# Performance work log

Measured on AMD Instinct MI355X. Metric: run time of the kernel, lower is better.

## Reference

```python
import jax, jax.numpy as jnp
import numpy as np

H = 2048      # hidden_size
K = 16        # n_memory_tokens
NQ = K + 2    # extraction queries (+halt, +value)
NH = 4        # extraction heads
HD = H // NH  # head dim = 512
FFN = 2 * H   # ffn_mult=2
MAXE = 128    # memory buffer capacity (full -> eviction path)
B, S = 4, 4096
EPS = 1e-6


def setup_inputs() -> dict:
    key = jax.random.key(0)
    ks = jax.random.split(key, 20)
    r = lambda i, shape, s=0.02: jax.random.normal(ks[i], shape, jnp.float32) * s
    return {
        "hidden_states": jax.random.normal(ks[0], (B, S, H), jnp.float32),
        "buf_entries": jax.random.normal(ks[1], (MAXE, H), jnp.float32),
        "buf_priorities": jax.random.uniform(ks[2], (MAXE,), jnp.float32),
        "queries": r(3, (NQ, H)),
        "Wq": r(4, (H, H)), "Wk": r(5, (H, H)), "Wv": r(6, (H, H)), "Wo": r(7, (H, H)),
        "ln_w": jnp.ones((H,), jnp.float32),
        "Wgate": r(8, (FFN, H)), "Wup": r(9, (FFN, H)), "Wdown": r(10, (H, FFN)),
        "Wp": r(11, (1, H)), "bp": jnp.full((1,), 0.5, jnp.float32),
        "Wh": r(12, (1, H)), "bh": jnp.full((1,), 1.0, jnp.float32),
        "V1": r(13, (H, 2 * H)), "b1": jnp.zeros((H,), jnp.float32),
        "V2": r(14, (H // 4, H)), "b2": jnp.zeros((H // 4,), jnp.float32),
        "V3": jnp.zeros((1, H // 4), jnp.float32), "b3": jnp.zeros((1,), jnp.float32),
    }


def reference(hidden_states, buf_entries, buf_priorities, queries,
              Wq, Wk, Wv, Wo, ln_w, Wgate, Wup, Wdown,
              Wp, bp, Wh, bh, V1, b1, V2, b2, V3, b3):
    b = hidden_states.shape[0]
    # --- cross-attention: NQ learned queries attend over hidden states ---
    q = (queries @ Wq.T).reshape(NQ, NH, HD)               # queries shared across batch
    k = (hidden_states @ Wk.T).reshape(b, -1, NH, HD)      # (b, s, h, d)
    v = (hidden_states @ Wv.T).reshape(b, -1, NH, HD)
    scores = jnp.einsum('qhd,bshd->bhqs', q, k) / jnp.sqrt(jnp.float32(HD))
    attn = jax.nn.softmax(scores, axis=-1)
    out = jnp.einsum('bhqs,bshd->bqhd', attn, v).reshape(b, NQ, H)
    extracted = out @ Wo.T
    memory_raw = extracted[:, :K]            # (b, K, H)
    confidence_vec = extracted[:, K]         # (b, H)
    value_vec = extracted[:, K + 1]          # (b, H)
    # --- RMSNorm + SwiGLU FFN residual (dropout = identity in eval) ---
    ms = jnp.mean(memory_raw * memory_raw, axis=-1, keepdims=True)
    xn = memory_raw * jax.lax.rsqrt(ms + EPS) * ln_w
    ffn = (jax.nn.silu(xn @ Wgate.T) * (xn @ Wup.T)) @ Wdown.T
    memory = memory_raw + ffn
    # --- heads ---
    priority = jax.nn.sigmoid(memory @ Wp.T + bp)[..., 0]          # (b, K)
    confidence = jax.nn.sigmoid(confidence_vec @ Wh.T + bh)[..., 0]  # (b,)
    value_input = jnp.concatenate([value_vec, hidden_states[:, -1, :]], axis=-1)
    h1 = jax.nn.silu(value_input @ V1.T + b1)
    h2 = jax.nn.silu(h1 @ V2.T + b2)
    value = (h2 @ V3.T + b3)[..., 0]                               # (b,)
    # --- MemoryBuffer.store with full buffer: sequential priority eviction ---
    # (torch loops K times with argmin().item() host syncs; lax.scan preserves
    #  the sequential compare-and-replace semantics in one fused program)
    vecs = jax.lax.stop_gradient(memory[0])     # store detaches; uses batch 0
    pris = jax.lax.stop_gradient(priority[0])

    def step(carry, xp):
        ent, pr = carry
        vec, p = xp
        idx = jnp.argmin(pr)
        take = p > pr[idx]
        ent = ent.at[idx].set(jnp.where(take, vec, ent[idx]))
        pr = pr.at[idx].set(jnp.where(take, p, pr[idx]))
        return (ent, pr), None

    (new_entries, new_priorities), _ = jax.lax.scan(step, (buf_entries, buf_priorities), (vecs, pris))
    return memory, priority, confidence, value, new_entries, new_priorities
```

## Files before the change

kernel.cpp:

```cpp
#include <hip/hip_runtime.h>

#define SS    4096
#define HH    2048
#define NQQ   18
#define QH    72
#define SCALE_F 0.044194173824159216f

#define OUT_MEM     0
#define OUT_PRI     131072
#define OUT_CONF    131136
#define OUT_VAL     131140
#define OUT_ENT     131144
#define OUT_NEWPRI  393288

typedef float  f32x4  __attribute__((ext_vector_type(4)));
typedef __bf16 bf16x8 __attribute__((ext_vector_type(8)));

#define DEVFN static __device__ __forceinline__

DEVFN bf16x8 pack8(f32x4 lo, f32x4 hi){
  bf16x8 r;
  #pragma unroll
  for (int i = 0; i < 4; i++){ r[i] = (__bf16)lo[i]; r[i+4] = (__bf16)hi[i]; }
  return r;
}
DEVFN float siluf(float x){ return x / (1.f + expf(-x)); }
DEVFN float block_sum(float v, float* sb){
  #pragma unroll
  for (int o = 32; o > 0; o >>= 1) v += __shfl_xor(v, o);
  int wid = threadIdx.x >> 6, lane = threadIdx.x & 63;
  if (lane == 0) sb[wid] = v;
  __syncthreads();
  v = sb[0] + sb[1] + sb[2] + sb[3];
  __syncthreads();
  return v;
}

template<int MF, int KC, bool HSEL>
__global__ __launch_bounds__(256) void gemm_bt(
    const __bf16* __restrict__ A, int Kf,
    const float* __restrict__ B0, float* __restrict__ C0,
    const float* __restrict__ B1, float* __restrict__ C1,
    int N)
{
  constexpr int Mp = 16 * MF;
  const int lane = threadIdx.x & 63, w = threadIdx.x >> 6;
  const int n0 = blockIdx.x * 64 + w * 16;
  const int k0 = blockIdx.y * KC * 32;
  const float* B = blockIdx.z ? B1 : B0;
  float* Cp      = blockIdx.z ? C1 : C0;
  const __bf16* aBase = A + (HSEL ? (long)(n0 >> 9) * Mp * Kf : 0)
                          + (long)(lane & 15) * Kf + k0 + 8 * (lane >> 4);
  const float* bBase = B + (long)(n0 + (lane & 15)) * Kf + k0 + 8 * (lane >> 4);
  f32x4 acc[MF];
  #pragma unroll
  for (int m = 0; m < MF; m++) acc[m] = (f32x4)(0.f);
  #pragma unroll 4
  for (int c = 0; c < KC; c++){
    f32x4 lo = *reinterpret_cast<const f32x4*>(bBase + c * 32);
    f32x4 hi = *reinterpret_cast<const f32x4*>(bBase + c * 32 + 4);
    bf16x8 bb = pack8(lo, hi);
    #pragma unroll
    for (int m = 0; m < MF; m++){
      bf16x8 aa = *reinterpret_cast<const bf16x8*>(aBase + (long)m * 16 * Kf + c * 32);
      acc[m] = __builtin_amdgcn_mfma_f32_16x16x32_bf16(aa, bb, acc[m], 0, 0, 0);
    }
  }
  float* cp = Cp + (long)blockIdx.y * Mp * N;
  int row0 = 4 * (lane >> 4), col = n0 + (lane & 15);
  #pragma unroll
  for (int m = 0; m < MF; m++)
    #pragma unroll
    for (int r = 0; r < 4; r++)
      cp[(long)(m * 16 + row0 + r) * N + col] = acc[m][r];
}

template<int MF, int KC>
__global__ __launch_bounds__(256) void gemm_abnat(
    const __bf16* __restrict__ A, long aBatch, int aStride,
    const float* __restrict__ Bn, long bBatch,
    float* __restrict__ Cp, long cBatch,
    int N)
{
  constexpr int Mp = 16 * MF;
  const int lane = threadIdx.x & 63, w = threadIdx.x >> 6;
  const int z = blockIdx.z;
  const int n0 = blockIdx.x * 64 + w * 16;
  const int k0 = blockIdx.y * KC * 32;
  const __bf16* aBase = A + z * aBatch + (long)(lane & 15) * aStride + k0 + 8 * (lane >> 4);
  const float* bBase = Bn + z * bBatch + (long)(k0 + 8 * (lane >> 4)) * N + n0 + (lane & 15);
  f32x4 acc[MF];
  #pragma unroll
  for (int m = 0; m < MF; m++) acc[m] = (f32x4)(0.f);
  #pragma unroll 2
  for (int c = 0; c < KC; c++){
    const float* bp = bBase + (long)c * 32 * N;
    bf16x8 bb;
    #pragma unroll
    for (int j = 0; j < 8; j++) bb[j] = (__bf16)bp[(long)j * N];
    #pragma unroll
    for (int m = 0; m < MF; m++){
      bf16x8 aa = *reinterpret_cast<const bf16x8*>(aBase + (long)m * 16 * aStride + c * 32);
      acc[m] = __builtin_amdgcn_mfma_f32_16x16x32_bf16(aa, bb, acc[m], 0, 0, 0);
    }
  }
  float* cp = Cp + z * cBatch + (long)blockIdx.y * Mp * N;
  int row0 = 4 * (lane >> 4), col = n0 + (lane & 15);
  #pragma unroll
  for (int m = 0; m < MF; m++)
    #pragma unroll
    for (int r = 0; r < 4; r++)
      cp[(long)(m * 16 + row0 + r) * N + col] = acc[m][r];
}

template<int KC>
__global__ __launch_bounds__(256) void gemm_pass1(
    const float* __restrict__ hs, const __bf16* __restrict__ qk,
    float* __restrict__ Sp)
{
  const int lane = threadIdx.x & 63, w = threadIdx.x >> 6;
  const int b = blockIdx.z;
  const int s0 = blockIdx.x * 64 + w * 16;
  const int k0 = blockIdx.y * KC * 32;
  const float* aBase = hs + ((long)b * SS + s0 + (lane & 15)) * HH + k0 + 8 * (lane >> 4);
  const __bf16* bBase = qk + (long)(lane & 15) * HH + k0 + 8 * (lane >> 4);
  f32x4 acc[5];
  #pragma unroll
  for (int n = 0; n < 5; n++) acc[n] = (f32x4)(0.f);
  #pragma unroll 4
  for (int c = 0; c < KC; c++){
    f32x4 lo = *reinterpret_cast<const f32x4*>(aBase + c * 32);
    f32x4 hi = *reinterpret_cast<const f32x4*>(aBase + c * 32 + 4);
    bf16x8 aa = pack8(lo, hi);
    #pragma unroll
    for (int n = 0; n < 5; n++){
      bf16x8 bb = *reinterpret_cast<const bf16x8*>(bBase + (long)n * 16 * HH + c * 32);
      acc[n] = __builtin_amdgcn_mfma_f32_16x16x32_bf16(aa, bb, acc[n], 0, 0, 0);
    }
  }
  float* sp = Sp + ((long)blockIdx.y * 4 + b) * 80 * SS;
  int scol = s0 + 4 * (lane >> 4);
  #pragma unroll
  for (int n = 0; n < 5; n++){
    int qh = n * 16 + (lane & 15);
    *reinterpret_cast<f32x4*>(sp + (long)qh * SS + scol) = acc[n];
  }
}

__global__ void k_prep_qA(const float* __restrict__ queries, __bf16* __restrict__ qA){
  int i = blockIdx.x * 256 + threadIdx.x;
  int r = i >> 11;
  qA[i] = (__bf16)((r < NQQ) ? queries[i] : 0.f);
}
__global__ void k_mkQ2(const float* __restrict__ q_p, __bf16* __restrict__ Q2){
  int i = blockIdx.x * 256 + threadIdx.x;
  int qh = i >> 11, e = i & 2047;
  float v = 0.f;
  if (qh < QH){
    int h = qh / NQQ, qq = qh - h * NQQ;
    if ((e >> 9) == h){
      float s = 0.f;
      #pragma unroll
      for (int y = 0; y < 8; y++) s += q_p[(long)y * 32 * 2048 + qq * 2048 + e];
      v = s * SCALE_F;
    }
  }
  Q2[i] = (__bf16)v;
}
__global__ void k_mkqk(const float* __restrict__ qk_p, __bf16* __restrict__ qk_bf){
  int i = blockIdx.x * 256 + threadIdx.x;
  float s = 0.f;
  #pragma unroll
  for (int y = 0; y < 8; y++) s += qk_p[(long)y * 80 * 2048 + i];
  qk_bf[i] = (__bf16)s;
}
__global__ __launch_bounds__(256) void k_softmax(const float* __restrict__ Sp, __bf16* __restrict__ attn){
  int qh = blockIdx.x, b = blockIdx.y;
  __bf16* arow = attn + ((long)b * 80 + qh) * SS;
  if (qh >= QH){
    #pragma unroll
    for (int it = 0; it < 16; it++) arow[threadIdx.x + 256 * it] = (__bf16)0.f;
    return;
  }
  const float* r0 = Sp + ((long)b * 80 + qh) * SS;
  const float* r1 = r0 + (long)4 * 80 * SS;
  float x[16]; float mx = -1e30f;
  #pragma unroll
  for (int it = 0; it < 16; it++){
    int s = threadIdx.x + 256 * it;
    x[it] = r0[s] + r1[s];
    mx = fmaxf(mx, x[it]);
  }
  __shared__ float sb[8];
  #pragma unroll
  for (int o = 32; o > 0; o >>= 1) mx = fmaxf(mx, __shfl_xor(mx, o));
  int wid = threadIdx.x >> 6, lane = threadIdx.x & 63;
  if (lane == 0) sb[wid] = mx;
  __syncthreads();
  mx = fmaxf(fmaxf(sb[0], sb[1]), fmaxf(sb[2], sb[3]));
  float sum = 0.f;
  #pragma unroll
  for (int it = 0; it < 16; it++){ x[it] = expf(x[it] - mx); sum += x[it]; }
  #pragma unroll
  for (int o = 32; o > 0; o >>= 1) sum += __shfl_xor(sum, o);
  if (lane == 0) sb[4 + wid] = sum;
  __syncthreads();
  sum = sb[4] + sb[5] + sb[6] + sb[7];
  float inv = 1.f / sum;
  #pragma unroll
  for (int it = 0; it < 16; it++) arow[threadIdx.x + 256 * it] = (__bf16)(x[it] * inv);
}
__global__ void k_pack_wv(const float* __restrict__ w_p, __bf16* __restrict__ Apack){
  int i = blockIdx.x * 256 + threadIdx.x;
  int h = i / (80 * 2048);
  int r = (i / 2048) % 80;
  int e = i & 2047;
  float v = 0.f;
  if (r < QH){
    int b = r / NQQ, qq = r - b * NQQ;
    const float* base = w_p + ((long)b * 4 * 80 + (h * NQQ + qq)) * 2048 + e;
    #pragma unroll
    for (int y = 0; y < 4; y++) v += base[(long)y * 80 * 2048];
  }
  Apack[i] = (__bf16)v;
}
__global__ void k_sum_outB(const float* __restrict__ outB_p, __bf16* __restrict__ outB){
  int i = blockIdx.x * 256 + threadIdx.x;
  float s = 0.f;
  #pragma unroll
  for (int y = 0; y < 8; y++) s += outB_p[(long)y * 80 * 2048 + i];
  outB[i] = (__bf16)s;
}
__global__ __launch_bounds__(256) void k_rms(const float* __restrict__ ext_p, const float* __restrict__ ln_w,
                                             float* __restrict__ extracted, __bf16* __restrict__ xnb){
  int r = blockIdx.x;
  if (r >= 80){
    __bf16* dst = xnb + (long)(r - 16) * HH;
    for (int i = threadIdx.x; i < HH; i += 256) dst[i] = (__bf16)0.f;
    return;
  }
  float xv[8]; float ss = 0.f;
  #pragma unroll
  for (int it = 0; it < 8; it++){
    int e = threadIdx.x + 256 * it;
    float s = 0.f;
    #pragma unroll
    for (int y = 0; y < 8; y++) s += ext_p[((long)y * 80 + r) * 2048 + e];
    extracted[(long)r * 2048 + e] = s;
    xv[it] = s;
    ss += s * s;
  }
  int b = r / NQQ, qq = r - b * NQQ;
  if (r < QH && qq < 16){
    __shared__ float sb[4];
    ss = block_sum(ss, sb);
    float inv = 1.f / sqrtf(ss * (1.f / 2048.f) + 1e-6f);
    __bf16* dst = xnb + (long)(b * 16 + qq) * HH;
    #pragma unroll
    for (int it = 0; it < 8; it++){
      int e = threadIdx.x + 256 * it;
      dst[e] = (__bf16)(xv[it] * inv * ln_w[e]);
    }
  }
}
__global__ void k_vi_pack(const float* __restrict__ extracted, const float* __restrict__ hs,
                          __bf16* __restrict__ vi){
  int i = blockIdx.x * 256 + threadIdx.x;
  int r = i >> 12, c = i & 4095;
  float v = 0.f;
  if (r < 4)
    v = (c < HH) ? extracted[(long)(r * NQQ + 17) * HH + c]
                 : hs[((long)r * SS + (SS - 1)) * HH + (c - HH)];
  vi[i] = (__bf16)v;
}
__global__ void k_act(const float* __restrict__ gate_p, const float* __restrict__ up_p,
                      __bf16* __restrict__ hb){
  int i = blockIdx.x * 256 + threadIdx.x;
  float g = 0.f, u = 0.f;
  #pragma unroll
  for (int y = 0; y < 4; y++){
    g += gate_p[(long)y * 80 * 4096 + i];
    u += up_p[(long)y * 80 * 4096 + i];
  }
  hb[i] = (__bf16)(siluf(g) * u);
}
__global__ void k_h1act(const float* __restrict__ h1_p, const float* __restrict__ b1,
                        __bf16* __restrict__ h1s){
  int i = blockIdx.x * 256 + threadIdx.x;
  int r = i >> 11, e = i & 2047;
  float v = 0.f;
  if (r < 4){
    float s = 0.f;
    #pragma unroll
    for (int y = 0; y < 16; y++) s += h1_p[(long)y * 16 * 2048 + i];
    v = siluf(s + b1[e]);
  }
  h1s[i] = (__bf16)v;
}
__global__ void k_memory(const float* __restrict__ extracted, const float* __restrict__ ffn_p,
                         float* __restrict__ out){
  int i = blockIdx.x * 256 + threadIdx.x;
  int b = i >> 15, qq = (i >> 11) & 15, e = i & 2047;
  float f = 0.f;
  #pragma unroll
  for (int y = 0; y < 8; y++) f += ffn_p[((long)y * 80 + b * 16 + qq) * 2048 + e];
  out[OUT_MEM + i] = extracted[(long)(b * NQQ + qq) * HH + e] + f;
}
__global__ __launch_bounds__(256) void k_heads(
    const float* __restrict__ out_ro, const float* __restrict__ extracted,
    const float* __restrict__ h2_p,
    const float* __restrict__ Wp, const float* __restrict__ bp,
    const float* __restrict__ Wh, const float* __restrict__ bh,
    const float* __restrict__ b2, const float* __restrict__ V3, const float* __restrict__ b3,
    float* __restrict__ out)
{
  __shared__ float sb[4];
  int blk = blockIdx.x;
  if (blk < 64){
    const float* m = out_ro + OUT_MEM + (long)blk * HH;
    float v = 0.f;
    #pragma unroll
    for (int it = 0; it < 8; it++){ int e = threadIdx.x + 256 * it; v += m[e] * Wp[e]; }
    v = block_sum(v, sb);
    if (threadIdx.x == 0) out[OUT_PRI + blk] = 1.f / (1.f + expf(-(v + bp[0])));
  } else if (blk < 68){
    int b = blk - 64;
    const float* m = extracted + (long)(b * NQQ + 16) * HH;
    float v = 0.f;
    #pragma unroll
    for (int it = 0; it < 8; it++){ int e = threadIdx.x + 256 * it; v += m[e] * Wh[e]; }
    v = block_sum(v, sb);
    if (threadIdx.x == 0) out[OUT_CONF + b] = 1.f / (1.f + expf(-(v + bh[0])));
  } else {
    int b = blk - 68;
    float v = 0.f;
    #pragma unroll
    for (int it = 0; it < 2; it++){
      int j = threadIdx.x + 256 * it;
      float s = 0.f;
      #pragma unroll
      for (int y = 0; y < 8; y++) s += h2_p[(long)y * 16 * 512 + b * 512 + j];
      v += siluf(s + b2[j]) * V3[j];
    }
    v = block_sum(v, sb);
    if (threadIdx.x == 0) out[OUT_VAL + b] = v + b3[0];
  }
}
__global__ void k_scan(const float* __restrict__ buf_pri, const float* __restrict__ out_ro,
                       float* __restrict__ out, int* __restrict__ tw){
  int lane = threadIdx.x;
  float pr0 = buf_pri[lane], pr1 = buf_pri[lane + 64];
  int tw0 = -1, tw1 = -1;
  for (int i = 0; i < 16; i++){
    float p = out_ro[OUT_PRI + i];
    float v; int idx;
    if (pr0 <= pr1){ v = pr0; idx = lane; } else { v = pr1; idx = lane + 64; }
    #pragma unroll
    for (int o = 32; o > 0; o >>= 1){
      float ov = __shfl_xor(v, o);
      int   oi = __shfl_xor(idx, o);
      if (ov < v || (ov == v && oi < idx)){ v = ov; idx = oi; }
    }
    if (p > v){
      if (idx == lane)          { pr0 = p; tw0 = i; }
      else if (idx == lane + 64){ pr1 = p; tw1 = i; }
    }
  }
  out[OUT_NEWPRI + lane]      = pr0;
  out[OUT_NEWPRI + lane + 64] = pr1;
  tw[lane] = tw0; tw[lane + 64] = tw1;
}
__global__ void k_entries(const float* __restrict__ buf_ent, const float* __restrict__ out_ro,
                          const int* __restrict__ tw, float* __restrict__ out){
  int row = blockIdx.x;
  int t = tw[row];
  const f32x4* s = reinterpret_cast<const f32x4*>(
      (t < 0) ? (buf_ent + (long)row * HH) : (out_ro + OUT_MEM + (long)t * HH));
  f32x4* d = reinterpret_cast<f32x4*>(out + OUT_ENT + (long)row * HH);
  #pragma unroll
  for (int i = 0; i < 2; i++) d[threadIdx.x + 256 * i] = s[threadIdx.x + 256 * i];
}

extern "C" void kernel_launch(void* const* d_in, const int* in_sizes, int n_in,
                              void* d_out, int out_size, void* d_ws, size_t ws_size,
                              hipStream_t stream)
{
  const float* hs      = (const float*)d_in[0];
  const float* buf_ent = (const float*)d_in[1];
  const float* buf_pri = (const float*)d_in[2];
  const float* queries = (const float*)d_in[3];
  const float* Wq  = (const float*)d_in[4];
  const float* Wk  = (const float*)d_in[5];
  const float* Wv  = (const float*)d_in[6];
  const float* Wo  = (const float*)d_in[7];
  const float* ln_w= (const float*)d_in[8];
  const float* Wgate=(const float*)d_in[9];
  const float* Wup = (const float*)d_in[10];
  const float* Wdown=(const float*)d_in[11];
  const float* Wp  = (const float*)d_in[12];
  const float* bp  = (const float*)d_in[13];
  const float* Wh  = (const float*)d_in[14];
  const float* bh  = (const float*)d_in[15];
  const float* V1  = (const float*)d_in[16];
  const float* b1  = (const float*)d_in[17];
  const float* V2  = (const float*)d_in[18];
  const float* b2  = (const float*)d_in[19];
  const float* V3  = (const float*)d_in[20];
  const float* b3  = (const float*)d_in[21];
  float* out = (float*)d_out;
  char* ws = (char*)d_ws;

  float* scores_p = (float*)(ws + 0);
  float* w_p      = (float*)(ws + 0);
  float* gate_p   = (float*)(ws + 0);
  float* up_p     = (float*)(ws + 5242880);
  float* q_p      = (float*)(ws + 10485760);
  float* qk_p     = (float*)(ws + 10485760);
  float* outB_p   = (float*)(ws + 10485760);
  float* ext_p    = (float*)(ws + 10485760);
  float* ffn_p    = (float*)(ws + 10485760);
  __bf16* qA    = (__bf16*)(ws + 15728640);
  __bf16* Q2    = (__bf16*)(ws + 15859712);
  __bf16* qk_bf = (__bf16*)(ws + 16187392);
  __bf16* attn  = (__bf16*)(ws + 16515072);
  __bf16* Apack = (__bf16*)(ws + 19136512);
  __bf16* outB  = (__bf16*)(ws + 20447232);
  float*  extracted = (float*)(ws + 20774912);
  __bf16* xnb   = (__bf16*)(ws + 21430272);
  __bf16* hb    = (__bf16*)(ws + 21757952);
  __bf16* vi    = (__bf16*)(ws + 22413312);
  __bf16* h1s   = (__bf16*)(ws + 22544384);
  float*  h1_p  = (float*)(ws + 22609920);
  float*  h2_p  = (float*)(ws + 24707072);
  int*    tw    = (int*)  (ws + 24969216);

  k_prep_qA<<<256, 256, 0, stream>>>(queries, qA);
  gemm_bt<2, 8, false><<<dim3(32, 8, 1), 256, 0, stream>>>(qA, 2048, Wq, q_p, Wq, q_p, 2048);
  k_mkQ2<<<640, 256, 0, stream>>>(q_p, Q2);
  gemm_abnat<5, 8><<<dim3(32, 8, 1), 256, 0, stream>>>(Q2, 0, 2048, Wk, 0, qk_p, 0, 2048);
  k_mkqk<<<640, 256, 0, stream>>>(qk_p, qk_bf);
  gemm_pass1<32><<<dim3(64, 2, 4), 256, 0, stream>>>(hs, qk_bf, scores_p);
  k_softmax<<<dim3(80, 4), 256, 0, stream>>>(scores_p, attn);
  gemm_abnat<5, 32><<<dim3(32, 4, 4), 256, 0, stream>>>(attn, 80L * 4096, 4096,
      hs, (long)SS * HH, w_p, 4L * 80 * 2048, 2048);
  k_pack_wv<<<2560, 256, 0, stream>>>(w_p, Apack);
  gemm_bt<5, 8, true><<<dim3(32, 8, 1), 256, 0, stream>>>(Apack, 2048, Wv, outB_p, Wv, outB_p, 2048);
  k_sum_outB<<<640, 256, 0, stream>>>(outB_p, outB);
  gemm_bt<5, 8, false><<<dim3(32, 8, 1), 256, 0, stream>>>(outB, 2048, Wo, ext_p, Wo, ext_p, 2048);
  k_rms<<<96, 256, 0, stream>>>(ext_p, ln_w, extracted, xnb);
  k_vi_pack<<<256, 256, 0, stream>>>(extracted, hs, vi);
  gemm_bt<5, 16, false><<<dim3(64, 4, 2), 256, 0, stream>>>(xnb, 2048, Wgate, gate_p, Wup, up_p, 4096);
  gemm_bt<1, 8, false><<<dim3(32, 16, 1), 256, 0, stream>>>(vi, 4096, V1, h1_p, V1, h1_p, 2048);
  k_act<<<1280, 256, 0, stream>>>(gate_p, up_p, hb);
  k_h1act<<<128, 256, 0, stream>>>(h1_p, b1, h1s);
  gemm_bt<5, 16, false><<<dim3(32, 8, 1), 256, 0, stream>>>(hb, 4096, Wdown, ffn_p, Wdown, ffn_p, 2048);
  gemm_bt<1, 8, false><<<dim3(8, 8, 1), 256, 0, stream>>>(h1s, 2048, V2, h2_p, V2, h2_p, 512);
  k_memory<<<512, 256, 0, stream>>>(extracted, ffn_p, out);
  k_heads<<<72, 256, 0, stream>>>(out, extracted, h2_p, Wp, bp, Wh, bh, b2, V3, b3, out);
  k_scan<<<1, 64, 0, stream>>>(buf_pri, out, out, tw);
  k_entries<<<128, 256, 0, stream>>>(buf_ent, out, tw, out);
}
```

Baseline: 313.2 us.

## Retune split-K factors, fuse vi packing into RMS and memory into heads

```diff
diff --git a/kernel.cpp b/kernel.cpp
--- a/kernel.cpp
+++ b/kernel.cpp
@@ -161,7 +161,7 @@
     if ((e >> 9) == h){
       float s = 0.f;
       #pragma unroll
-      for (int y = 0; y < 8; y++) s += q_p[(long)y * 32 * 2048 + qq * 2048 + e];
+      for (int y = 0; y < 16; y++) s += q_p[(long)y * 32 * 2048 + qq * 2048 + e];
       v = s * SCALE_F;
     }
   }
@@ -171,7 +171,7 @@
   int i = blockIdx.x * 256 + threadIdx.x;
   float s = 0.f;
   #pragma unroll
-  for (int y = 0; y < 8; y++) s += qk_p[(long)y * 80 * 2048 + i];
+  for (int y = 0; y < 16; y++) s += qk_p[(long)y * 80 * 2048 + i];
   qk_bf[i] = (__bf16)s;
 }
 __global__ __launch_bounds__(256) void k_softmax(const float* __restrict__ Sp, __bf16* __restrict__ attn){
@@ -183,12 +183,12 @@
     return;
   }
   const float* r0 = Sp + ((long)b * 80 + qh) * SS;
-  const float* r1 = r0 + (long)4 * 80 * SS;
+  const long ys = (long)4 * 80 * SS;
   float x[16]; float mx = -1e30f;
   #pragma unroll
   for (int it = 0; it < 16; it++){
     int s = threadIdx.x + 256 * it;
-    x[it] = r0[s] + r1[s];
+    x[it] = (r0[s] + r0[s + ys]) + (r0[s + 2 * ys] + r0[s + 3 * ys]);
     mx = fmaxf(mx, x[it]);
   }
   __shared__ float sb[8];
@@ -218,9 +218,9 @@
   float v = 0.f;
   if (r < QH){
     int b = r / NQQ, qq = r - b * NQQ;
-    const float* base = w_p + ((long)b * 4 * 80 + (h * NQQ + qq)) * 2048 + e;
-    #pragma unroll
-    for (int y = 0; y < 4; y++) v += base[(long)y * 80 * 2048];
+    const float* base = w_p + ((long)b * 8 * 80 + (h * NQQ + qq)) * 2048 + e;
+    #pragma unroll
+    for (int y = 0; y < 8; y++) v += base[(long)y * 80 * 2048];
   }
   Apack[i] = (__bf16)v;
 }
@@ -228,15 +228,29 @@
   int i = blockIdx.x * 256 + threadIdx.x;
   float s = 0.f;
   #pragma unroll
-  for (int y = 0; y < 8; y++) s += outB_p[(long)y * 80 * 2048 + i];
+  for (int y = 0; y < 16; y++) s += outB_p[(long)y * 80 * 2048 + i];
   outB[i] = (__bf16)s;
 }
 __global__ __launch_bounds__(256) void k_rms(const float* __restrict__ ext_p, const float* __restrict__ ln_w,
-                                             float* __restrict__ extracted, __bf16* __restrict__ xnb){
+                                             const float* __restrict__ hs,
+                                             float* __restrict__ extracted, __bf16* __restrict__ xnb,
+                                             __bf16* __restrict__ vi){
   int r = blockIdx.x;
   if (r >= 80){
-    __bf16* dst = xnb + (long)(r - 16) * HH;
-    for (int i = threadIdx.x; i < HH; i += 256) dst[i] = (__bf16)0.f;
+    if (r < 84){
+      int b = r - 80;
+      const float* src = hs + ((long)b * SS + (SS - 1)) * HH;
+      #pragma unroll
+      for (int it = 0; it < 8; it++){
+        int e = threadIdx.x + 256 * it;
+        vi[(long)b * 4096 + 2048 + e] = (__bf16)src[e];
+      }
+    } else {
+      int row = 4 + (r - 84);
+      #pragma unroll
+      for (int it = 0; it < 16; it++)
+        vi[(long)row * 4096 + threadIdx.x + 256 * it] = (__bf16)0.f;
+    }
     return;
   }
   float xv[8]; float ss = 0.f;
@@ -245,13 +259,14 @@
     int e = threadIdx.x + 256 * it;
     float s = 0.f;
     #pragma unroll
-    for (int y = 0; y < 8; y++) s += ext_p[((long)y * 80 + r) * 2048 + e];
+    for (int y = 0; y < 16; y++) s += ext_p[((long)y * 80 + r) * 2048 + e];
     extracted[(long)r * 2048 + e] = s;
     xv[it] = s;
     ss += s * s;
   }
+  if (r >= QH) return;
   int b = r / NQQ, qq = r - b * NQQ;
-  if (r < QH && qq < 16){
+  if (qq < 16){
     __shared__ float sb[4];
     ss = block_sum(ss, sb);
     float inv = 1.f / sqrtf(ss * (1.f / 2048.f) + 1e-6f);
@@ -261,17 +276,13 @@
       int e = threadIdx.x + 256 * it;
       dst[e] = (__bf16)(xv[it] * inv * ln_w[e]);
     }
-  }
-}
-__global__ void k_vi_pack(const float* __restrict__ extracted, const float* __restrict__ hs,
-                          __bf16* __restrict__ vi){
-  int i = blockIdx.x * 256 + threadIdx.x;
-  int r = i >> 12, c = i & 4095;
-  float v = 0.f;
-  if (r < 4)
-    v = (c < HH) ? extracted[(long)(r * NQQ + 17) * HH + c]
-                 : hs[((long)r * SS + (SS - 1)) * HH + (c - HH)];
-  vi[i] = (__bf16)v;
+  } else if (qq == 17){
+    #pragma unroll
+    for (int it = 0; it < 8; it++){
+      int e = threadIdx.x + 256 * it;
+      vi[(long)b * 4096 + e] = (__bf16)xv[it];
+    }
+  }
 }
 __global__ void k_act(const float* __restrict__ gate_p, const float* __restrict__ up_p,
                       __bf16* __restrict__ hb){
@@ -279,8 +290,8 @@
   float g = 0.f, u = 0.f;
   #pragma unroll
   for (int y = 0; y < 4; y++){
-    g += gate_p[(long)y * 80 * 4096 + i];
-    u += up_p[(long)y * 80 * 4096 + i];
+    g += gate_p[(long)y * 64 * 4096 + i];
+    u += up_p[(long)y * 64 * 4096 + i];
   }
   hb[i] = (__bf16)(siluf(g) * u);
 }
@@ -297,17 +308,8 @@
   }
   h1s[i] = (__bf16)v;
 }
-__global__ void k_memory(const float* __restrict__ extracted, const float* __restrict__ ffn_p,
-                         float* __restrict__ out){
-  int i = blockIdx.x * 256 + threadIdx.x;
-  int b = i >> 15, qq = (i >> 11) & 15, e = i & 2047;
-  float f = 0.f;
-  #pragma unroll
-  for (int y = 0; y < 8; y++) f += ffn_p[((long)y * 80 + b * 16 + qq) * 2048 + e];
-  out[OUT_MEM + i] = extracted[(long)(b * NQQ + qq) * HH + e] + f;
-}
-__global__ __launch_bounds__(256) void k_heads(
-    const float* __restrict__ out_ro, const float* __restrict__ extracted,
+__global__ __launch_bounds__(256) void k_epilogue(
+    const float* __restrict__ extracted, const float* __restrict__ ffn_p,
     const float* __restrict__ h2_p,
     const float* __restrict__ Wp, const float* __restrict__ bp,
     const float* __restrict__ Wh, const float* __restrict__ bh,
@@ -317,12 +319,21 @@
   __shared__ float sb[4];
   int blk = blockIdx.x;
   if (blk < 64){
-    const float* m = out_ro + OUT_MEM + (long)blk * HH;
-    float v = 0.f;
-    #pragma unroll
-    for (int it = 0; it < 8; it++){ int e = threadIdx.x + 256 * it; v += m[e] * Wp[e]; }
-    v = block_sum(v, sb);
-    if (threadIdx.x == 0) out[OUT_PRI + blk] = 1.f / (1.f + expf(-(v + bp[0])));
+    int b = blk >> 4, qq = blk & 15;
+    const float* ext = extracted + (long)(b * NQQ + qq) * HH;
+    float pv = 0.f;
+    #pragma unroll
+    for (int it = 0; it < 8; it++){
+      int e = threadIdx.x + 256 * it;
+      float f = 0.f;
+      #pragma unroll
+      for (int y = 0; y < 8; y++) f += ffn_p[((long)y * 64 + blk) * 2048 + e];
+      float m = ext[e] + f;
+      out[OUT_MEM + (long)blk * 2048 + e] = m;
+      pv += m * Wp[e];
+    }
+    pv = block_sum(pv, sb);
+    if (threadIdx.x == 0) out[OUT_PRI + blk] = 1.f / (1.f + expf(-(pv + bp[0])));
   } else if (blk < 68){
     int b = blk - 64;
     const float* m = extracted + (long)(b * NQQ + 16) * HH;
@@ -339,7 +350,7 @@
       int j = threadIdx.x + 256 * it;
       float s = 0.f;
       #pragma unroll
-      for (int y = 0; y < 8; y++) s += h2_p[(long)y * 16 * 512 + b * 512 + j];
+      for (int y = 0; y < 16; y++) s += h2_p[(long)y * 16 * 512 + b * 512 + j];
       v += siluf(s + b2[j]) * V3[j];
     }
     v = block_sum(v, sb);
@@ -410,53 +421,51 @@
   float* out = (float*)d_out;
   char* ws = (char*)d_ws;
 
+  float* q_p      = (float*)(ws + 0);
+  float* qk_p     = (float*)(ws + 0);
   float* scores_p = (float*)(ws + 0);
   float* w_p      = (float*)(ws + 0);
+  float* outB_p   = (float*)(ws + 0);
+  float* ext_p    = (float*)(ws + 0);
   float* gate_p   = (float*)(ws + 0);
-  float* up_p     = (float*)(ws + 5242880);
-  float* q_p      = (float*)(ws + 10485760);
-  float* qk_p     = (float*)(ws + 10485760);
-  float* outB_p   = (float*)(ws + 10485760);
-  float* ext_p    = (float*)(ws + 10485760);
-  float* ffn_p    = (float*)(ws + 10485760);
-  __bf16* qA    = (__bf16*)(ws + 15728640);
-  __bf16* Q2    = (__bf16*)(ws + 15859712);
-  __bf16* qk_bf = (__bf16*)(ws + 16187392);
-  __bf16* attn  = (__bf16*)(ws + 16515072);
-  __bf16* Apack = (__bf16*)(ws + 19136512);
-  __bf16* outB  = (__bf16*)(ws + 20447232);
-  float*  extracted = (float*)(ws + 20774912);
-  __bf16* xnb   = (__bf16*)(ws + 21430272);
-  __bf16* hb    = (__bf16*)(ws + 21757952);
-  __bf16* vi    = (__bf16*)(ws + 22413312);
-  __bf16* h1s   = (__bf16*)(ws + 22544384);
-  float*  h1_p  = (float*)(ws + 22609920);
-  float*  h2_p  = (float*)(ws + 24707072);
-  int*    tw    = (int*)  (ws + 24969216);
+  float* up_p     = (float*)(ws + 4194304);
+  float* ffn_p    = (float*)(ws + 0);
+  __bf16* qA    = (__bf16*)(ws + 20971520);
+  __bf16* Q2    = (__bf16*)(ws + 21102592);
+  __bf16* qk_bf = (__bf16*)(ws + 21430272);
+  __bf16* attn  = (__bf16*)(ws + 21757952);
+  __bf16* Apack = (__bf16*)(ws + 24379392);
+  __bf16* outB  = (__bf16*)(ws + 25690112);
+  float*  extracted = (float*)(ws + 26017792);
+  __bf16* xnb   = (__bf16*)(ws + 26673152);
+  __bf16* hb    = (__bf16*)(ws + 26935296);
+  __bf16* vi    = (__bf16*)(ws + 27459584);
+  __bf16* h1s   = (__bf16*)(ws + 27590656);
+  float*  h1_p  = (float*)(ws + 27656192);
+  float*  h2_p  = (float*)(ws + 29753344);
+  int*    tw    = (int*)  (ws + 30277632);
 
   k_prep_qA<<<256, 256, 0, stream>>>(queries, qA);
-  gemm_bt<2, 8, false><<<dim3(32, 8, 1), 256, 0, stream>>>(qA, 2048, Wq, q_p, Wq, q_p, 2048);
+  gemm_bt<2, 4, false><<<dim3(32, 16, 1), 256, 0, stream>>>(qA, 2048, Wq, q_p, Wq, q_p, 2048);
   k_mkQ2<<<640, 256, 0, stream>>>(q_p, Q2);
-  gemm_abnat<5, 8><<<dim3(32, 8, 1), 256, 0, stream>>>(Q2, 0, 2048, Wk, 0, qk_p, 0, 2048);
+  gemm_abnat<5, 4><<<dim3(32, 16, 1), 256, 0, stream>>>(Q2, 0, 2048, Wk, 0, qk_p, 0, 2048);
   k_mkqk<<<640, 256, 0, stream>>>(qk_p, qk_bf);
-  gemm_pass1<32><<<dim3(64, 2, 4), 256, 0, stream>>>(hs, qk_bf, scores_p);
+  gemm_pass1<16><<<dim3(64, 4, 4), 256, 0, stream>>>(hs, qk_bf, scores_p);
   k_softmax<<<dim3(80, 4), 256, 0, stream>>>(scores_p, attn);
-  gemm_abnat<5, 32><<<dim3(32, 4, 4), 256, 0, stream>>>(attn, 80L * 4096, 4096,
-      hs, (long)SS * HH, w_p, 4L * 80 * 2048, 2048);
+  gemm_abnat<5, 16><<<dim3(32, 8, 4), 256, 0, stream>>>(attn, 80L * 4096, 4096,
+      hs, (long)SS * HH, w_p, 8L * 80 * 2048, 2048);
   k_pack_wv<<<2560, 256, 0, stream>>>(w_p, Apack);
-  gemm_bt<5, 8, true><<<dim3(32, 8, 1), 256, 0, stream>>>(Apack, 2048, Wv, outB_p, Wv, outB_p, 2048);
+  gemm_bt<5, 4, true><<<dim3(32, 16, 1), 256, 0, stream>>>(Apack, 2048, Wv, outB_p, Wv, outB_p, 2048);
   k_sum_outB<<<640, 256, 0, stream>>>(outB_p, outB);
-  gemm_bt<5, 8, false><<<dim3(32, 8, 1), 256, 0, stream>>>(outB, 2048, Wo, ext_p, Wo, ext_p, 2048);
-  k_rms<<<96, 256, 0, stream>>>(ext_p, ln_w, extracted, xnb);
-  k_vi_pack<<<256, 256, 0, stream>>>(extracted, hs, vi);
-  gemm_bt<5, 16, false><<<dim3(64, 4, 2), 256, 0, stream>>>(xnb, 2048, Wgate, gate_p, Wup, up_p, 4096);
+  gemm_bt<5, 4, false><<<dim3(32, 16, 1), 256, 0, stream>>>(outB, 2048, Wo, ext_p, Wo, ext_p, 2048);
+  k_rms<<<96, 256, 0, stream>>>(ext_p, ln_w, hs, extracted, xnb, vi);
+  gemm_bt<4, 16, false><<<dim3(64, 4, 2), 256, 0, stream>>>(xnb, 2048, Wgate, gate_p, Wup, up_p, 4096);
   gemm_bt<1, 8, false><<<dim3(32, 16, 1), 256, 0, stream>>>(vi, 4096, V1, h1_p, V1, h1_p, 2048);
-  k_act<<<1280, 256, 0, stream>>>(gate_p, up_p, hb);
+  k_act<<<1024, 256, 0, stream>>>(gate_p, up_p, hb);
   k_h1act<<<128, 256, 0, stream>>>(h1_p, b1, h1s);
-  gemm_bt<5, 16, false><<<dim3(32, 8, 1), 256, 0, stream>>>(hb, 4096, Wdown, ffn_p, Wdown, ffn_p, 2048);
-  gemm_bt<1, 8, false><<<dim3(8, 8, 1), 256, 0, stream>>>(h1s, 2048, V2, h2_p, V2, h2_p, 512);
-  k_memory<<<512, 256, 0, stream>>>(extracted, ffn_p, out);
-  k_heads<<<72, 256, 0, stream>>>(out, extracted, h2_p, Wp, bp, Wh, bh, b2, V3, b3, out);
+  gemm_bt<4, 16, false><<<dim3(32, 8, 1), 256, 0, stream>>>(hb, 4096, Wdown, ffn_p, Wdown, ffn_p, 2048);
+  gemm_bt<1, 4, false><<<dim3(8, 16, 1), 256, 0, stream>>>(h1s, 2048, V2, h2_p, V2, h2_p, 512);
+  k_epilogue<<<72, 256, 0, stream>>>(extracted, ffn_p, h2_p, Wp, bp, Wh, bh, b2, V3, b3, out);
   k_scan<<<1, 64, 0, stream>>>(buf_pri, out, out, tw);
   k_entries<<<128, 256, 0, stream>>>(buf_ent, out, tw, out);
 }
```

New measurement: 282.2 us. 1.11x faster.
